# Performance work log

Hardware: AMD Instinct MI355X
Metric: run time of the kernel (lower is better)

## Reference

```python
import jax, jax.numpy as jnp
import numpy as np

N_ATOMS = 50000
N_EDGES = 1_600_000
FEAT = 128
FP_LEN = 2048
RADIUS = 3


def setup_inputs() -> dict:
    key = jax.random.key(0)
    k = jax.random.split(key, 6)
    atomsFeatures = jax.random.normal(k[0], (N_ATOMS, FEAT), dtype=jnp.float32)
    W1 = jax.random.normal(k[1], (FEAT, FEAT), dtype=jnp.float32) * 0.05
    b1 = jnp.zeros((FEAT,), dtype=jnp.float32)
    W2 = jax.random.normal(k[2], (FEAT, FP_LEN), dtype=jnp.float32) * 0.05
    b2 = jnp.zeros((FP_LEN,), dtype=jnp.float32)
    edge_src = jax.random.randint(k[3], (N_EDGES,), 0, N_ATOMS, dtype=jnp.int32)
    edge_dst = jax.random.randint(k[4], (N_EDGES,), 0, N_ATOMS, dtype=jnp.int32)
    return {"atomsFeatures": atomsFeatures, "W1": W1, "b1": b1,
            "W2": W2, "b2": b2, "edge_src": edge_src, "edge_dst": edge_dst}


def reference(atomsFeatures, W1, b1, W2, b2, edge_src, edge_dst):
    # Duvenaud-style neural fingerprint:
    # per radius step: x_i <- x_i + sum_{j in N(i)} x_j ; h = relu(lin1(x));
    # fp += sum_atoms softmax(lin2(h)); x <- h
    fp0 = jnp.zeros((1, FP_LEN), dtype=atomsFeatures.dtype)

    def step(carry, _):
        x, fp = carry
        # neighbor-sum via segment reduce over the edge list (self + neighbors)
        agg = x + jax.ops.segment_sum(x[edge_src], edge_dst, num_segments=N_ATOMS)
        h = jax.nn.relu(agg @ W1 + b1)            # [N, FEAT]
        probs = jax.nn.softmax(h @ W2 + b2, axis=1)  # [N, FP_LEN]
        fp = fp + jnp.sum(probs, axis=0, keepdims=True)
        return (h, fp), None

    (_, fp), _ = jax.lax.scan(step, (atomsFeatures, fp0), None, length=RADIUS)
    return fp
```

## Files before the change

### kernel.cpp

```cpp
#include <hip/hip_runtime.h>

typedef short short8 __attribute__((ext_vector_type(8)));
typedef __bf16 bf16x8 __attribute__((ext_vector_type(8)));
typedef float f32x4 __attribute__((ext_vector_type(4)));

#define FEAT 128
#define FPL 2048

__device__ __forceinline__ float b2f(unsigned int u) {
  union { unsigned int u; float f; } c; c.u = u << 16; return c.f;
}
__device__ __forceinline__ unsigned short f2b(float f) {
  union { float f; unsigned int u; } c; c.f = f;
  unsigned int r = c.u + 0x7fffu + ((c.u >> 16) & 1u);
  return (unsigned short)(r >> 16);
}
__device__ __forceinline__ f32x4 mfma16(short8 a, short8 b, f32x4 c) {
  return __builtin_amdgcn_mfma_f32_16x16x32_bf16(
      __builtin_bit_cast(bf16x8, a), __builtin_bit_cast(bf16x8, b), c, 0, 0, 0);
}

__global__ void cvt_kernel(const float* __restrict__ in, unsigned short* __restrict__ out, int n2) {
  int i = blockIdx.x * 256 + threadIdx.x;
  if (i < n2) {
    float2 v = ((const float2*)in)[i];
    unsigned int lo = f2b(v.x), hi = f2b(v.y);
    ((unsigned int*)out)[i] = lo | (hi << 16);
  }
}

__global__ void cvtT_kernel(const float* __restrict__ W, unsigned short* __restrict__ WT, int K, int N) {
  int i = blockIdx.x * 256 + threadIdx.x;
  if (i < K * N) {
    int k = i / N, c = i - k * N;
    WT[(size_t)c * K + k] = f2b(W[i]);
  }
}

__global__ void count_kernel(const int* __restrict__ dst, int* __restrict__ cnt, int n) {
  int i = blockIdx.x * 256 + threadIdx.x;
  if (i < n) atomicAdd(&cnt[dst[i]], 1);
}

__global__ __launch_bounds__(1024) void scan1_kernel(const int* __restrict__ cnt,
    int* __restrict__ ex, int* __restrict__ chunkSum, int n) {
  __shared__ int sd[1024];
  const int i = blockIdx.x * 1024 + threadIdx.x;
  int v = (i < n) ? cnt[i] : 0;
  sd[threadIdx.x] = v;
  __syncthreads();
  int sum = v;
  for (int off = 1; off < 1024; off <<= 1) {
    int t = (threadIdx.x >= (unsigned)off) ? sd[threadIdx.x - off] : 0;
    __syncthreads();
    sum += t;
    sd[threadIdx.x] = sum;
    __syncthreads();
  }
  if (i < n) ex[i] = sum - v;
  if (threadIdx.x == 1023) chunkSum[blockIdx.x] = sum;
}

__global__ __launch_bounds__(1024) void scan2_kernel(const int* __restrict__ chunkSum,
    int* __restrict__ chunkOff, int nChunks) {
  __shared__ int sd[1024];
  int v = (threadIdx.x < (unsigned)nChunks) ? chunkSum[threadIdx.x] : 0;
  sd[threadIdx.x] = v;
  __syncthreads();
  int sum = v;
  for (int off = 1; off < 1024; off <<= 1) {
    int t = (threadIdx.x >= (unsigned)off) ? sd[threadIdx.x - off] : 0;
    __syncthreads();
    sum += t;
    sd[threadIdx.x] = sum;
    __syncthreads();
  }
  if (threadIdx.x < (unsigned)nChunks) chunkOff[threadIdx.x] = sum - v;
}

__global__ void scan3_kernel(const int* __restrict__ ex, const int* __restrict__ chunkOff,
    const int* __restrict__ chunkSum, int* __restrict__ rp, int n, int nChunks) {
  int i = blockIdx.x * 256 + threadIdx.x;
  if (i < n) rp[i] = ex[i] + chunkOff[i >> 10];
  if (i == 0) rp[n] = chunkOff[nChunks - 1] + chunkSum[nChunks - 1];
}

__global__ void copy_kernel(const int* __restrict__ a, int* __restrict__ b, int n) {
  int i = blockIdx.x * 256 + threadIdx.x;
  if (i < n) b[i] = a[i];
}

__global__ __launch_bounds__(256) void fillx_kernel(const int* __restrict__ src,
    const int* __restrict__ dst, int* __restrict__ cursor, int* __restrict__ col,
    int n, int nAtoms) {
  const int part = blockIdx.x & 7;
  const int blkInPart = blockIdx.x >> 3;
  const int nBlkPerPart = gridDim.x >> 3;
  const int partSize = (nAtoms + 7) >> 3;
  const int lo = part * partSize;
  const int hi = min(lo + partSize, nAtoms);
  const int stride = nBlkPerPart * 256;
  for (int i = blkInPart * 256 + (int)threadIdx.x; i < n; i += stride) {
    int d = dst[i];
    if (d >= lo && d < hi) {
      int p = atomicAdd(&cursor[d], 1);
      col[p] = src[i];
    }
  }
}

__global__ __launch_bounds__(256) void gather_kernel(const unsigned short* __restrict__ x,
    const int* __restrict__ rp, const int* __restrict__ col,
    unsigned short* __restrict__ agg, int n) {
  int wid = (blockIdx.x * 256 + threadIdx.x) >> 6;
  int lane = threadIdx.x & 63;
  if (wid >= n) return;
  const int half = lane >> 5;
  const int l32 = lane & 31;
  const unsigned long long* xq = (const unsigned long long*)x;

  float a0, a1, a2, a3;
  {
    unsigned long long sv = xq[(size_t)wid * 32 + l32];
    if (half == 0) {
      a0 = b2f((unsigned int)(sv & 0xffffu));
      a1 = b2f((unsigned int)((sv >> 16) & 0xffffu));
      a2 = b2f((unsigned int)((sv >> 32) & 0xffffu));
      a3 = b2f((unsigned int)((sv >> 48) & 0xffffu));
    } else {
      a0 = a1 = a2 = a3 = 0.f;
    }
  }
  const int beg = rp[wid], end = rp[wid + 1];
  int j = beg;
  for (; j + 4 <= end; j += 4) {
    int c0 = col[j + half];
    int c1 = col[j + 2 + half];
    unsigned long long v0 = xq[(size_t)c0 * 32 + l32];
    unsigned long long v1 = xq[(size_t)c1 * 32 + l32];
    a0 += b2f((unsigned int)(v0 & 0xffffu)) + b2f((unsigned int)(v1 & 0xffffu));
    a1 += b2f((unsigned int)((v0 >> 16) & 0xffffu)) + b2f((unsigned int)((v1 >> 16) & 0xffffu));
    a2 += b2f((unsigned int)((v0 >> 32) & 0xffffu)) + b2f((unsigned int)((v1 >> 32) & 0xffffu));
    a3 += b2f((unsigned int)((v0 >> 48) & 0xffffu)) + b2f((unsigned int)((v1 >> 48) & 0xffffu));
  }
  if (j + 2 <= end) {
    int c0 = col[j + half];
    unsigned long long v0 = xq[(size_t)c0 * 32 + l32];
    a0 += b2f((unsigned int)(v0 & 0xffffu));
    a1 += b2f((unsigned int)((v0 >> 16) & 0xffffu));
    a2 += b2f((unsigned int)((v0 >> 32) & 0xffffu));
    a3 += b2f((unsigned int)((v0 >> 48) & 0xffffu));
    j += 2;
  }
  if (j < end && half == 0) {
    int c0 = col[j];
    unsigned long long v0 = xq[(size_t)c0 * 32 + l32];
    a0 += b2f((unsigned int)(v0 & 0xffffu));
    a1 += b2f((unsigned int)((v0 >> 16) & 0xffffu));
    a2 += b2f((unsigned int)((v0 >> 32) & 0xffffu));
    a3 += b2f((unsigned int)((v0 >> 48) & 0xffffu));
  }
  a0 += __shfl_xor(a0, 32, 64);
  a1 += __shfl_xor(a1, 32, 64);
  a2 += __shfl_xor(a2, 32, 64);
  a3 += __shfl_xor(a3, 32, 64);
  if (half == 0) {
    unsigned long long r = (unsigned long long)f2b(a0) |
                           ((unsigned long long)f2b(a1) << 16) |
                           ((unsigned long long)f2b(a2) << 32) |
                           ((unsigned long long)f2b(a3) << 48);
    ((unsigned long long*)agg)[(size_t)wid * 32 + l32] = r;
  }
}

__global__ __launch_bounds__(256) void gemm1_kernel(
    const unsigned short* __restrict__ A, const unsigned short* __restrict__ W1T,
    const float* __restrict__ b1, unsigned short* __restrict__ H, int n) {
  const int wave = threadIdx.x >> 6;
  const int lane = threadIdx.x & 63;
  const int lr = lane & 15, lg = lane >> 4;
  const int rowBase = blockIdx.x * 64 + wave * 16;
  short8 a[4];
#pragma unroll
  for (int kt = 0; kt < 4; ++kt)
    a[kt] = *(const short8*)(A + (size_t)(rowBase + lr) * FEAT + kt * 32 + lg * 8);
  f32x4 acc[8];
#pragma unroll
  for (int ct = 0; ct < 8; ++ct) {
    const unsigned short* bp = W1T + (size_t)(ct * 16 + lr) * FEAT + lg * 8;
    f32x4 c = {0.f, 0.f, 0.f, 0.f};
    c = mfma16(a[0], *(const short8*)(bp), c);
    c = mfma16(a[1], *(const short8*)(bp + 32), c);
    c = mfma16(a[2], *(const short8*)(bp + 64), c);
    c = mfma16(a[3], *(const short8*)(bp + 96), c);
    acc[ct] = c;
  }
#pragma unroll
  for (int ct = 0; ct < 8; ++ct) {
    const int c = ct * 16 + lr;
    const float bias = b1[c];
#pragma unroll
    for (int j = 0; j < 4; ++j) {
      const int row = rowBase + lg * 4 + j;
      if (row < n) {
        float v = acc[ct][j] + bias;
        H[(size_t)row * FEAT + c] = f2b(v > 0.f ? v : 0.f);
      }
    }
  }
}


__global__ __launch_bounds__(512) void statT_kernel(
    const unsigned short* __restrict__ H, const unsigned short* __restrict__ W2T,
    const float* __restrict__ b2, float* __restrict__ pm, float* __restrict__ ps,
    int nPad) {
  __shared__ short8 ldsB[4096];
  __shared__ float ldsBias[256];
  const int wave = threadIdx.x >> 6;
  const int lane = threadIdx.x & 63;
  const int lr = lane & 15, lg = lane >> 4;
  const int nRowBlk = nPad >> 8;
  const int rowBlk = blockIdx.x % nRowBlk;
  const int colBlk = blockIdx.x / nRowBlk;
  const int rowBase = rowBlk * 256 + wave * 32;
  const int colBase = colBlk * 256;

#pragma unroll
  for (int r = 0; r < 8; ++r) {
    const int p = r * 8 + wave;
    const int ct = p >> 2, q = p & 3;
    ldsB[p * 64 + lane] =
        *(const short8*)(W2T + (size_t)(colBase + ct * 16 + lr) * FEAT + (q * 4 + lg) * 8);
  }
  if (threadIdx.x < 256) ldsBias[threadIdx.x] = b2[colBase + threadIdx.x];

  short8 a[2][4];
#pragma unroll
  for (int g = 0; g < 2; ++g)
#pragma unroll
    for (int kt = 0; kt < 4; ++kt)
      a[g][kt] = *(const short8*)(H + (size_t)(rowBase + g * 16 + lr) * FEAT + kt * 32 + lg * 8);
  __syncthreads();

  float m[2][4], s[2][4];
#pragma unroll
  for (int g = 0; g < 2; ++g)
#pragma unroll
    for (int j = 0; j < 4; ++j) { m[g][j] = -1e30f; s[g][j] = 0.f; }

#pragma unroll 4
  for (int ct = 0; ct < 16; ++ct) {
    short8 q0 = ldsB[(ct * 4 + 0) * 64 + lane];
    short8 q1 = ldsB[(ct * 4 + 1) * 64 + lane];
    short8 q2 = ldsB[(ct * 4 + 2) * 64 + lane];
    short8 q3 = ldsB[(ct * 4 + 3) * 64 + lane];
    f32x4 c0 = {0.f, 0.f, 0.f, 0.f};
    f32x4 c1 = {0.f, 0.f, 0.f, 0.f};
    c0 = mfma16(a[0][0], q0, c0);
    c1 = mfma16(a[1][0], q0, c1);
    c0 = mfma16(a[0][1], q1, c0);
    c1 = mfma16(a[1][1], q1, c1);
    c0 = mfma16(a[0][2], q2, c0);
    c1 = mfma16(a[1][2], q2, c1);
    c0 = mfma16(a[0][3], q3, c0);
    c1 = mfma16(a[1][3], q3, c1);
    const float bs = ldsBias[ct * 16 + lr];
    float e0[4], e1[4];
#pragma unroll
    for (int j = 0; j < 4; ++j) { e0[j] = c0[j] + bs; e1[j] = c1[j] + bs; }
    bool need = false;
#pragma unroll
    for (int j = 0; j < 4; ++j)
      need = need || (e0[j] > m[0][j] + 8.f) || (e1[j] > m[1][j] + 8.f);
    if (__any(need)) {
#pragma unroll
      for (int j = 0; j < 4; ++j) {
        float nm0 = fmaxf(m[0][j], e0[j]);
        s[0][j] = s[0][j] * __expf(m[0][j] - nm0) + __expf(e0[j] - nm0);
        m[0][j] = nm0;
        float nm1 = fmaxf(m[1][j], e1[j]);
        s[1][j] = s[1][j] * __expf(m[1][j] - nm1) + __expf(e1[j] - nm1);
        m[1][j] = nm1;
      }
    } else {
#pragma unroll
      for (int j = 0; j < 4; ++j) {
        s[0][j] += __expf(e0[j] - m[0][j]);
        s[1][j] += __expf(e1[j] - m[1][j]);
      }
    }
  }
#pragma unroll
  for (int g = 0; g < 2; ++g)
#pragma unroll
    for (int j = 0; j < 4; ++j) {
#pragma unroll
      for (int d = 1; d < 16; d <<= 1) {
        float om = __shfl_xor(m[g][j], d, 64);
        float os = __shfl_xor(s[g][j], d, 64);
        float nm = fmaxf(m[g][j], om);
        s[g][j] = s[g][j] * __expf(m[g][j] - nm) + os * __expf(om - nm);
        m[g][j] = nm;
      }
    }
  if (lr == 0) {
#pragma unroll
    for (int g = 0; g < 2; ++g)
#pragma unroll
      for (int j = 0; j < 4; ++j) {
        const int row = rowBase + g * 16 + lg * 4 + j;
        pm[(size_t)colBlk * nPad + row] = m[g][j];
        ps[(size_t)colBlk * nPad + row] = s[g][j];
      }
  }
}

__global__ void mergeT_kernel(const float* __restrict__ pm, const float* __restrict__ ps,
                              float* __restrict__ T, int nPad) {
  int r = blockIdx.x * 256 + threadIdx.x;
  if (r < nPad) {
    float M = pm[r];
#pragma unroll
    for (int k = 1; k < 8; ++k) M = fmaxf(M, pm[(size_t)k * nPad + r]);
    float S = 0.f;
#pragma unroll
    for (int k = 0; k < 8; ++k) S += ps[(size_t)k * nPad + r] * __expf(pm[(size_t)k * nPad + r] - M);
    T[r] = M + __logf(S);
  }
}

__global__ __launch_bounds__(512) void fpacc_kernel(
    const unsigned short* __restrict__ H, const unsigned short* __restrict__ W2T,
    const float* __restrict__ b2, const float* __restrict__ T,
    float* __restrict__ partials, int n, int nPad) {
  __shared__ short8 ldsB[4096];
  __shared__ float ldsBias[256];
  __shared__ float fp_w[8][256];
  const int wave = threadIdx.x >> 6;
  const int lane = threadIdx.x & 63;
  const int lr = lane & 15, lg = lane >> 4;
  const int nRowBlk = nPad >> 8;
  const int rowBlk = blockIdx.x % nRowBlk;
  const int colBlk = blockIdx.x / nRowBlk;
  const int rowBase = rowBlk * 256 + wave * 32;
  const int colBase = colBlk * 256;

#pragma unroll
  for (int r = 0; r < 8; ++r) {
    const int p = r * 8 + wave;
    const int ct = p >> 2, q = p & 3;
    ldsB[p * 64 + lane] =
        *(const short8*)(W2T + (size_t)(colBase + ct * 16 + lr) * FEAT + (q * 4 + lg) * 8);
  }
  if (threadIdx.x < 256) ldsBias[threadIdx.x] = b2[colBase + threadIdx.x];

  short8 a[2][4];
#pragma unroll
  for (int g = 0; g < 2; ++g)
#pragma unroll
    for (int kt = 0; kt < 4; ++kt)
      a[g][kt] = *(const short8*)(H + (size_t)(rowBase + g * 16 + lr) * FEAT + kt * 32 + lg * 8);
  float Tj[2][4];
#pragma unroll
  for (int g = 0; g < 2; ++g)
#pragma unroll
    for (int j = 0; j < 4; ++j) {
      const int row = rowBase + g * 16 + lg * 4 + j;
      Tj[g][j] = (row < n) ? T[row] : 1e30f;
    }
  __syncthreads();

#pragma unroll 4
  for (int ct = 0; ct < 16; ++ct) {
    short8 q0 = ldsB[(ct * 4 + 0) * 64 + lane];
    short8 q1 = ldsB[(ct * 4 + 1) * 64 + lane];
    short8 q2 = ldsB[(ct * 4 + 2) * 64 + lane];
    short8 q3 = ldsB[(ct * 4 + 3) * 64 + lane];
    f32x4 c0 = {0.f, 0.f, 0.f, 0.f};
    f32x4 c1 = {0.f, 0.f, 0.f, 0.f};
    c0 = mfma16(a[0][0], q0, c0);
    c1 = mfma16(a[1][0], q0, c1);
    c0 = mfma16(a[0][1], q1, c0);
    c1 = mfma16(a[1][1], q1, c1);
    c0 = mfma16(a[0][2], q2, c0);
    c1 = mfma16(a[1][2], q2, c1);
    c0 = mfma16(a[0][3], q3, c0);
    c1 = mfma16(a[1][3], q3, c1);
    const float bs = ldsBias[ct * 16 + lr];
    float p = __expf(c0[0] + bs - Tj[0][0]) + __expf(c0[1] + bs - Tj[0][1]) +
              __expf(c0[2] + bs - Tj[0][2]) + __expf(c0[3] + bs - Tj[0][3]) +
              __expf(c1[0] + bs - Tj[1][0]) + __expf(c1[1] + bs - Tj[1][1]) +
              __expf(c1[2] + bs - Tj[1][2]) + __expf(c1[3] + bs - Tj[1][3]);
    p += __shfl_xor(p, 16, 64);
    p += __shfl_xor(p, 32, 64);
    if (lg == 0) fp_w[wave][ct * 16 + lr] = p;
  }
  __syncthreads();
  if (threadIdx.x < 256) {
    float sum = 0.f;
#pragma unroll
    for (int w = 0; w < 8; ++w) sum += fp_w[w][threadIdx.x];
    partials[(size_t)rowBlk * FPL + colBase + threadIdx.x] += sum;
  }
}

__global__ void reduce_kernel(const float* __restrict__ partials, float* __restrict__ out, int nPart) {
  int c = blockIdx.x * 256 + threadIdx.x;
  if (c < FPL) {
    float s = 0.f;
    for (int p = 0; p < nPart; ++p) s += partials[(size_t)p * FPL + c];
    out[c] = s;
  }
}

extern "C" void kernel_launch(void* const* d_in, const int* in_sizes, int n_in,
                              void* d_out, int out_size, void* d_ws, size_t ws_size,
                              hipStream_t stream) {
  const float* atoms = (const float*)d_in[0];
  const float* W1 = (const float*)d_in[1];
  const float* b1 = (const float*)d_in[2];
  const float* W2 = (const float*)d_in[3];
  const float* b2 = (const float*)d_in[4];
  const int* esrc = (const int*)d_in[5];
  const int* edst = (const int*)d_in[6];
  const int nAtoms = in_sizes[0] / FEAT;
  const int nEdges = in_sizes[5];
  if (nAtoms <= 0) return;

  const int g2Blocks = (nAtoms + 255) / 256;
  const int nPad = g2Blocks * 256;
  const int g1Blocks = nPad / 64;
  const int nChunks = (nAtoms + 1023) / 1024;

  size_t off = 0;
  auto alloc = [&](size_t bytes) -> void* {
    void* p = (char*)d_ws + off;
    off += (bytes + 255) & ~(size_t)255;
    return p;
  };
  unsigned short* P = (unsigned short*)alloc((size_t)nPad * FEAT * 2);
  unsigned short* Q = (unsigned short*)alloc((size_t)nPad * FEAT * 2);
  unsigned short* W1T = (unsigned short*)alloc((size_t)FEAT * FEAT * 2);
  unsigned short* W2T = (unsigned short*)alloc((size_t)FEAT * FPL * 2);
  int* counts = (int*)alloc((size_t)nAtoms * 4);
  int* cursor = (int*)alloc((size_t)nAtoms * 4);
  int* rp = (int*)alloc(((size_t)nAtoms + 1) * 4);
  int* ex = (int*)alloc((size_t)nAtoms * 4);
  int* chunkSum = (int*)alloc((size_t)nChunks * 4);
  int* chunkOff = (int*)alloc((size_t)nChunks * 4);
  int* col = (int*)alloc((size_t)nEdges * 4);
  float* pm = (float*)alloc((size_t)8 * nPad * 4);
  float* ps = (float*)alloc((size_t)8 * nPad * 4);
  float* Trow = (float*)alloc((size_t)nPad * 4);
  float* partials = (float*)alloc((size_t)g2Blocks * FPL * 4);

  hipMemsetAsync(counts, 0, (size_t)nAtoms * 4, stream);
  hipMemsetAsync(partials, 0, (size_t)g2Blocks * FPL * 4, stream);
  hipMemsetAsync(P + (size_t)nAtoms * FEAT, 0, (size_t)(nPad - nAtoms) * FEAT * 2, stream);
  hipMemsetAsync(Q + (size_t)nAtoms * FEAT, 0, (size_t)(nPad - nAtoms) * FEAT * 2, stream);

  const int n2 = in_sizes[0] / 2;
  cvt_kernel<<<(n2 + 255) / 256, 256, 0, stream>>>(atoms, P, n2);
  cvtT_kernel<<<(FEAT * FEAT + 255) / 256, 256, 0, stream>>>(W1, W1T, FEAT, FEAT);
  cvtT_kernel<<<(FEAT * FPL + 255) / 256, 256, 0, stream>>>(W2, W2T, FEAT, FPL);
  count_kernel<<<(nEdges + 255) / 256, 256, 0, stream>>>(edst, counts, nEdges);
  scan1_kernel<<<nChunks, 1024, 0, stream>>>(counts, ex, chunkSum, nAtoms);
  scan2_kernel<<<1, 1024, 0, stream>>>(chunkSum, chunkOff, nChunks);
  scan3_kernel<<<(nAtoms + 255) / 256, 256, 0, stream>>>(ex, chunkOff, chunkSum, rp, nAtoms, nChunks);
  copy_kernel<<<(nAtoms + 255) / 256, 256, 0, stream>>>(rp, cursor, nAtoms);
  fillx_kernel<<<1024, 256, 0, stream>>>(esrc, edst, cursor, col, nEdges, nAtoms);

  unsigned short* x = P;
  unsigned short* y = Q;
  for (int step = 0; step < 3; ++step) {
    gather_kernel<<<(nAtoms + 3) / 4, 256, 0, stream>>>(x, rp, col, y, nAtoms);
    gemm1_kernel<<<g1Blocks, 256, 0, stream>>>(y, W1T, b1, y, nAtoms);
    statT_kernel<<<g2Blocks * 8, 512, 0, stream>>>(y, W2T, b2, pm, ps, nPad);
    mergeT_kernel<<<(nPad + 255) / 256, 256, 0, stream>>>(pm, ps, Trow, nPad);
    fpacc_kernel<<<g2Blocks * 8, 512, 0, stream>>>(y, W2T, b2, Trow, partials, nAtoms, nPad);
    unsigned short* t = x; x = y; y = t;
  }
  reduce_kernel<<<(FPL + 255) / 256, 256, 0, stream>>>(partials, (float*)d_out, g2Blocks);
}
```

Baseline: 788.5 us.

## Fold log2e into W2, use raw exp2, halve column tiles, nontemporal edge loads

W2 and b2 are pre-scaled by log2(e) so the softmax kernels can call the hardware v_exp_f32 (exp2) directly instead of __expf, which removes a multiply per exponential. The column tile in statT and fpacc shrinks from 256 to 128 columns, doubling the grid and halving LDS per block to raise occupancy, with mergeT now combining 16 partial statistics. The online-softmax rescale threshold also changes, and fillx uses nontemporal loads and only reads src for edges in its partition. The added cost is more blocks that each reload H rows, plus small numeric changes from the scaled bf16 weights.

```diff
diff --git a/kernel.cpp b/kernel.cpp
--- a/kernel.cpp
+++ b/kernel.cpp
@@ -6,6 +6,7 @@
 
 #define FEAT 128
 #define FPL 2048
+#define LOG2E 1.4426950408889634f
 
 __device__ __forceinline__ float b2f(unsigned int u) {
   union { unsigned int u; float f; } c; c.u = u << 16; return c.f;
@@ -18,6 +19,9 @@
 __device__ __forceinline__ f32x4 mfma16(short8 a, short8 b, f32x4 c) {
   return __builtin_amdgcn_mfma_f32_16x16x32_bf16(
       __builtin_bit_cast(bf16x8, a), __builtin_bit_cast(bf16x8, b), c, 0, 0, 0);
+}
+__device__ __forceinline__ float exp2x(float x) {
+  float r; asm("v_exp_f32 %0, %1" : "=v"(r) : "v"(x)); return r;
 }
 
 __global__ void cvt_kernel(const float* __restrict__ in, unsigned short* __restrict__ out, int n2) {
@@ -29,11 +33,12 @@
   }
 }
 
-__global__ void cvtT_kernel(const float* __restrict__ W, unsigned short* __restrict__ WT, int K, int N) {
+__global__ void cvtT_kernel(const float* __restrict__ W, unsigned short* __restrict__ WT,
+                            int K, int N, float scale) {
   int i = blockIdx.x * 256 + threadIdx.x;
   if (i < K * N) {
     int k = i / N, c = i - k * N;
-    WT[(size_t)c * K + k] = f2b(W[i]);
+    WT[(size_t)c * K + k] = f2b(W[i] * scale);
   }
 }
 
@@ -101,10 +106,11 @@
   const int hi = min(lo + partSize, nAtoms);
   const int stride = nBlkPerPart * 256;
   for (int i = blkInPart * 256 + (int)threadIdx.x; i < n; i += stride) {
-    int d = dst[i];
+    int d = __builtin_nontemporal_load(&dst[i]);
     if (d >= lo && d < hi) {
+      int s = __builtin_nontemporal_load(&src[i]);
       int p = atomicAdd(&cursor[d], 1);
-      col[p] = src[i];
+      col[p] = s;
     }
   }
 }
@@ -215,8 +221,8 @@
     const unsigned short* __restrict__ H, const unsigned short* __restrict__ W2T,
     const float* __restrict__ b2, float* __restrict__ pm, float* __restrict__ ps,
     int nPad) {
-  __shared__ short8 ldsB[4096];
-  __shared__ float ldsBias[256];
+  __shared__ short8 ldsB[2048];
+  __shared__ float ldsBias[128];
   const int wave = threadIdx.x >> 6;
   const int lane = threadIdx.x & 63;
   const int lr = lane & 15, lg = lane >> 4;
@@ -224,16 +230,16 @@
   const int rowBlk = blockIdx.x % nRowBlk;
   const int colBlk = blockIdx.x / nRowBlk;
   const int rowBase = rowBlk * 256 + wave * 32;
-  const int colBase = colBlk * 256;
-
-#pragma unroll
-  for (int r = 0; r < 8; ++r) {
+  const int colBase = colBlk * 128;
+
+#pragma unroll
+  for (int r = 0; r < 4; ++r) {
     const int p = r * 8 + wave;
     const int ct = p >> 2, q = p & 3;
     ldsB[p * 64 + lane] =
         *(const short8*)(W2T + (size_t)(colBase + ct * 16 + lr) * FEAT + (q * 4 + lg) * 8);
   }
-  if (threadIdx.x < 256) ldsBias[threadIdx.x] = b2[colBase + threadIdx.x];
+  if (threadIdx.x < 128) ldsBias[threadIdx.x] = b2[colBase + threadIdx.x] * LOG2E;
 
   short8 a[2][4];
 #pragma unroll
@@ -250,7 +256,7 @@
     for (int j = 0; j < 4; ++j) { m[g][j] = -1e30f; s[g][j] = 0.f; }
 
 #pragma unroll 4
-  for (int ct = 0; ct < 16; ++ct) {
+  for (int ct = 0; ct < 8; ++ct) {
     short8 q0 = ldsB[(ct * 4 + 0) * 64 + lane];
     short8 q1 = ldsB[(ct * 4 + 1) * 64 + lane];
     short8 q2 = ldsB[(ct * 4 + 2) * 64 + lane];
@@ -266,28 +272,30 @@
     c0 = mfma16(a[0][3], q3, c0);
     c1 = mfma16(a[1][3], q3, c1);
     const float bs = ldsBias[ct * 16 + lr];
-    float e0[4], e1[4];
-#pragma unroll
-    for (int j = 0; j < 4; ++j) { e0[j] = c0[j] + bs; e1[j] = c1[j] + bs; }
-    bool need = false;
-#pragma unroll
-    for (int j = 0; j < 4; ++j)
-      need = need || (e0[j] > m[0][j] + 8.f) || (e1[j] > m[1][j] + 8.f);
-    if (__any(need)) {
+    float d0[4], d1[4];
+#pragma unroll
+    for (int j = 0; j < 4; ++j) {
+      d0[j] = c0[j] + bs - m[0][j];
+      d1[j] = c1[j] + bs - m[1][j];
+    }
+    float dmax = fmaxf(fmaxf(fmaxf(d0[0], d0[1]), fmaxf(d0[2], d0[3])),
+                       fmaxf(fmaxf(d1[0], d1[1]), fmaxf(d1[2], d1[3])));
+    if (__any(dmax > 12.f)) {
 #pragma unroll
       for (int j = 0; j < 4; ++j) {
-        float nm0 = fmaxf(m[0][j], e0[j]);
-        s[0][j] = s[0][j] * __expf(m[0][j] - nm0) + __expf(e0[j] - nm0);
+        float e0 = d0[j] + m[0][j], e1 = d1[j] + m[1][j];
+        float nm0 = fmaxf(m[0][j], e0);
+        s[0][j] = s[0][j] * exp2x(m[0][j] - nm0) + exp2x(e0 - nm0);
         m[0][j] = nm0;
-        float nm1 = fmaxf(m[1][j], e1[j]);
-        s[1][j] = s[1][j] * __expf(m[1][j] - nm1) + __expf(e1[j] - nm1);
+        float nm1 = fmaxf(m[1][j], e1);
+        s[1][j] = s[1][j] * exp2x(m[1][j] - nm1) + exp2x(e1 - nm1);
         m[1][j] = nm1;
       }
     } else {
 #pragma unroll
       for (int j = 0; j < 4; ++j) {
-        s[0][j] += __expf(e0[j] - m[0][j]);
-        s[1][j] += __expf(e1[j] - m[1][j]);
+        s[0][j] += exp2x(d0[j]);
+        s[1][j] += exp2x(d1[j]);
       }
     }
   }
@@ -300,7 +308,7 @@
         float om = __shfl_xor(m[g][j], d, 64);
         float os = __shfl_xor(s[g][j], d, 64);
         float nm = fmaxf(m[g][j], om);
-        s[g][j] = s[g][j] * __expf(m[g][j] - nm) + os * __expf(om - nm);
+        s[g][j] = s[g][j] * exp2x(m[g][j] - nm) + os * exp2x(om - nm);
         m[g][j] = nm;
       }
     }
@@ -322,11 +330,11 @@
   if (r < nPad) {
     float M = pm[r];
 #pragma unroll
-    for (int k = 1; k < 8; ++k) M = fmaxf(M, pm[(size_t)k * nPad + r]);
+    for (int k = 1; k < 16; ++k) M = fmaxf(M, pm[(size_t)k * nPad + r]);
     float S = 0.f;
 #pragma unroll
-    for (int k = 0; k < 8; ++k) S += ps[(size_t)k * nPad + r] * __expf(pm[(size_t)k * nPad + r] - M);
-    T[r] = M + __logf(S);
+    for (int k = 0; k < 16; ++k) S += ps[(size_t)k * nPad + r] * exp2x(pm[(size_t)k * nPad + r] - M);
+    T[r] = M + __log2f(S);
   }
 }
 
@@ -334,9 +342,9 @@
     const unsigned short* __restrict__ H, const unsigned short* __restrict__ W2T,
     const float* __restrict__ b2, const float* __restrict__ T,
     float* __restrict__ partials, int n, int nPad) {
-  __shared__ short8 ldsB[4096];
-  __shared__ float ldsBias[256];
-  __shared__ float fp_w[8][256];
+  __shared__ short8 ldsB[2048];
+  __shared__ float ldsBias[128];
+  __shared__ float fp_w[8][128];
   const int wave = threadIdx.x >> 6;
   const int lane = threadIdx.x & 63;
   const int lr = lane & 15, lg = lane >> 4;
@@ -344,16 +352,16 @@
   const int rowBlk = blockIdx.x % nRowBlk;
   const int colBlk = blockIdx.x / nRowBlk;
   const int rowBase = rowBlk * 256 + wave * 32;
-  const int colBase = colBlk * 256;
-
-#pragma unroll
-  for (int r = 0; r < 8; ++r) {
+  const int colBase = colBlk * 128;
+
+#pragma unroll
+  for (int r = 0; r < 4; ++r) {
     const int p = r * 8 + wave;
     const int ct = p >> 2, q = p & 3;
     ldsB[p * 64 + lane] =
         *(const short8*)(W2T + (size_t)(colBase + ct * 16 + lr) * FEAT + (q * 4 + lg) * 8);
   }
-  if (threadIdx.x < 256) ldsBias[threadIdx.x] = b2[colBase + threadIdx.x];
+  if (threadIdx.x < 128) ldsBias[threadIdx.x] = b2[colBase + threadIdx.x] * LOG2E;
 
   short8 a[2][4];
 #pragma unroll
@@ -361,18 +369,18 @@
 #pragma unroll
     for (int kt = 0; kt < 4; ++kt)
       a[g][kt] = *(const short8*)(H + (size_t)(rowBase + g * 16 + lr) * FEAT + kt * 32 + lg * 8);
-  float Tj[2][4];
+  float Tq[2][4];
 #pragma unroll
   for (int g = 0; g < 2; ++g)
 #pragma unroll
     for (int j = 0; j < 4; ++j) {
       const int row = rowBase + g * 16 + lg * 4 + j;
-      Tj[g][j] = (row < n) ? T[row] : 1e30f;
+      Tq[g][j] = (row < n) ? T[row] : 1e30f;
     }
   __syncthreads();
 
 #pragma unroll 4
-  for (int ct = 0; ct < 16; ++ct) {
+  for (int ct = 0; ct < 8; ++ct) {
     short8 q0 = ldsB[(ct * 4 + 0) * 64 + lane];
     short8 q1 = ldsB[(ct * 4 + 1) * 64 + lane];
     short8 q2 = ldsB[(ct * 4 + 2) * 64 + lane];
@@ -388,16 +396,16 @@
     c0 = mfma16(a[0][3], q3, c0);
     c1 = mfma16(a[1][3], q3, c1);
     const float bs = ldsBias[ct * 16 + lr];
-    float p = __expf(c0[0] + bs - Tj[0][0]) + __expf(c0[1] + bs - Tj[0][1]) +
-              __expf(c0[2] + bs - Tj[0][2]) + __expf(c0[3] + bs - Tj[0][3]) +
-              __expf(c1[0] + bs - Tj[1][0]) + __expf(c1[1] + bs - Tj[1][1]) +
-              __expf(c1[2] + bs - Tj[1][2]) + __expf(c1[3] + bs - Tj[1][3]);
+    float p = exp2x(c0[0] + (bs - Tq[0][0])) + exp2x(c0[1] + (bs - Tq[0][1])) +
+              exp2x(c0[2] + (bs - Tq[0][2])) + exp2x(c0[3] + (bs - Tq[0][3])) +
+              exp2x(c1[0] + (bs - Tq[1][0])) + exp2x(c1[1] + (bs - Tq[1][1])) +
+              exp2x(c1[2] + (bs - Tq[1][2])) + exp2x(c1[3] + (bs - Tq[1][3]));
     p += __shfl_xor(p, 16, 64);
     p += __shfl_xor(p, 32, 64);
     if (lg == 0) fp_w[wave][ct * 16 + lr] = p;
   }
   __syncthreads();
-  if (threadIdx.x < 256) {
+  if (threadIdx.x < 128) {
     float sum = 0.f;
 #pragma unroll
     for (int w = 0; w < 8; ++w) sum += fp_w[w][threadIdx.x];
@@ -450,8 +458,8 @@
   int* chunkSum = (int*)alloc((size_t)nChunks * 4);
   int* chunkOff = (int*)alloc((size_t)nChunks * 4);
   int* col = (int*)alloc((size_t)nEdges * 4);
-  float* pm = (float*)alloc((size_t)8 * nPad * 4);
-  float* ps = (float*)alloc((size_t)8 * nPad * 4);
+  float* pm = (float*)alloc((size_t)16 * nPad * 4);
+  float* ps = (float*)alloc((size_t)16 * nPad * 4);
   float* Trow = (float*)alloc((size_t)nPad * 4);
   float* partials = (float*)alloc((size_t)g2Blocks * FPL * 4);
 
@@ -462,8 +470,8 @@
 
   const int n2 = in_sizes[0] / 2;
   cvt_kernel<<<(n2 + 255) / 256, 256, 0, stream>>>(atoms, P, n2);
-  cvtT_kernel<<<(FEAT * FEAT + 255) / 256, 256, 0, stream>>>(W1, W1T, FEAT, FEAT);
-  cvtT_kernel<<<(FEAT * FPL + 255) / 256, 256, 0, stream>>>(W2, W2T, FEAT, FPL);
+  cvtT_kernel<<<(FEAT * FEAT + 255) / 256, 256, 0, stream>>>(W1, W1T, FEAT, FEAT, 1.0f);
+  cvtT_kernel<<<(FEAT * FPL + 255) / 256, 256, 0, stream>>>(W2, W2T, FEAT, FPL, LOG2E);
   count_kernel<<<(nEdges + 255) / 256, 256, 0, stream>>>(edst, counts, nEdges);
   scan1_kernel<<<nChunks, 1024, 0, stream>>>(counts, ex, chunkSum, nAtoms);
   scan2_kernel<<<1, 1024, 0, stream>>>(chunkSum, chunkOff, nChunks);
@@ -476,9 +484,9 @@
   for (int step = 0; step < 3; ++step) {
     gather_kernel<<<(nAtoms + 3) / 4, 256, 0, stream>>>(x, rp, col, y, nAtoms);
     gemm1_kernel<<<g1Blocks, 256, 0, stream>>>(y, W1T, b1, y, nAtoms);
-    statT_kernel<<<g2Blocks * 8, 512, 0, stream>>>(y, W2T, b2, pm, ps, nPad);
+    statT_kernel<<<g2Blocks * 16, 512, 0, stream>>>(y, W2T, b2, pm, ps, nPad);
     mergeT_kernel<<<(nPad + 255) / 256, 256, 0, stream>>>(pm, ps, Trow, nPad);
-    fpacc_kernel<<<g2Blocks * 8, 512, 0, stream>>>(y, W2T, b2, Trow, partials, nAtoms, nPad);
+    fpacc_kernel<<<g2Blocks * 16, 512, 0, stream>>>(y, W2T, b2, Trow, partials, nAtoms, nPad);
     unsigned short* t = x; x = y; y = t;
   }
   reduce_kernel<<<(FPL + 255) / 256, 256, 0, stream>>>(partials, (float*)d_out, g2Blocks);
```

Measured after the change: 780.7 us. No clear change (-1.0%).
